# Performance work log

Hardware: AMD Instinct MI355X
Metric: run time of the kernel (lower is better)

The kernel has to match this reference:

```python
import jax, jax.numpy as jnp
import numpy as np

K = 128      # num_topics
T = 256      # num_times
E = 320      # rho_size
H = 10       # num_heads (fixed in source)
HD = E // H  # head dim
TM1 = T - 1
EPS = 1e-5   # nn.LayerNorm default eps


def setup_inputs() -> dict:
    key = jax.random.key(0)
    ks = jax.random.split(key, 6)
    s = 0.02
    return {
        "mu_0_alpha": jax.random.normal(ks[0], (1, K, E), jnp.float32),
        "qkv_w": jax.random.normal(ks[1], (3 * E, E), jnp.float32) * s,
        "qkv_b": jnp.zeros((3 * E,), jnp.float32),
        "in_proj_w": jax.random.normal(ks[2], (3 * E, E), jnp.float32) * s,
        "in_proj_b": jnp.zeros((3 * E,), jnp.float32),
        "out_w": jax.random.normal(ks[3], (E, E), jnp.float32) * s,
        "out_b": jnp.zeros((E,), jnp.float32),
        "ln_g": jnp.ones((E,), jnp.float32),
        "ln_b": jnp.zeros((E,), jnp.float32),
    }


def _layer_norm(x, g, b):
    m = jnp.mean(x, axis=-1, keepdims=True)
    v = jnp.mean((x - m) ** 2, axis=-1, keepdims=True)
    return (x - m) * jax.lax.rsqrt(v + EPS) * g + b


def reference(mu_0_alpha, qkv_w, qkv_b, in_proj_w, in_proj_b, out_w, out_b, ln_g, ln_b):
    # nn.MultiheadAttention in-projection split (q/k/v same embed_dim)
    Wq, Wk, Wv = jnp.split(in_proj_w, 3, axis=0)   # each (E, E)
    bq, bk, bv = jnp.split(in_proj_b, 3, axis=0)
    scale = 1.0 / np.sqrt(HD)

    alpha0 = _layer_norm(mu_0_alpha[0], ln_g, ln_b)  # (K, E)
    kc0 = jnp.zeros((TM1 * K, E), jnp.float32)       # persistent projected-K cache
    vc0 = jnp.zeros((TM1 * K, E), jnp.float32)
    pos = jnp.arange(TM1 * K)

    def step(carry, idx):
        alpha, kc, vc = carry
        # per-step qkv_proj (the module's own Linear, before MHA's in-proj)
        qkv = alpha @ qkv_w.T + qkv_b                 # (K, 3E)
        q, k, v = jnp.split(qkv, 3, axis=-1)
        # MHA in-projections; store projected K/V in the cache (equivalent to
        # projecting the concatenated cache each step, since proj is per-row)
        q2 = (q @ Wq.T + bq) * scale                  # (K, E)
        k2 = k @ Wk.T + bk
        v2 = v @ Wv.T + bv
        kc = jax.lax.dynamic_update_slice(kc, k2, (idx * K, 0))
        vc = jax.lax.dynamic_update_slice(vc, v2, (idx * K, 0))
        qh = q2.reshape(K, H, HD).transpose(1, 0, 2)          # (H, K, HD)
        kh = kc.reshape(TM1 * K, H, HD).transpose(1, 0, 2)    # (H, S, HD)
        vh = vc.reshape(TM1 * K, H, HD).transpose(1, 0, 2)
        scores = jnp.einsum('hqd,hkd->hqk', qh, kh)           # (H, K, S)
        valid = pos < (idx + 1) * K                            # growing-KV mask
        scores = jnp.where(valid[None, None, :], scores, -1e30)
        w = jax.nn.softmax(scores, axis=-1)
        o = jnp.einsum('hqk,hkd->hqd', w, vh)                  # (H, K, HD)
        o = o.transpose(1, 0, 2).reshape(K, E) @ out_w.T + out_b
        new_alpha = _layer_norm(o + alpha, ln_g, ln_b)         # residual + LN
        return (new_alpha, kc, vc), new_alpha

    _, alphas_rest = jax.lax.scan(step, (alpha0, kc0, vc0), jnp.arange(TM1))
    return jnp.concatenate([alpha0[None], alphas_rest], axis=0)  # (T, K, E)
```

## Files before the change

kernel.cpp:

```cpp
#include <hip/hip_runtime.h>
#include <hip/hip_bf16.h>
#include <math.h>

typedef __hip_bfloat16 bf16;
using short4v = __attribute__((ext_vector_type(4))) short;
using short8 = __attribute__((ext_vector_type(8))) short;
using f32x4  = __attribute__((ext_vector_type(4))) float;

#define E_ 320
#define K_ 128
#define H_ 10
#define HD_ 32
#define T_ 256
#define TM1_ 255
#define SMAX_ (TM1_*K_)
#define MAXCH_ 25
#define NBLK_ 256
#define QSCALE 0.17677669529663687f
#define EPS_LN 1e-5f

#define LD1(d,p)  asm volatile("global_load_dword %0, %1, off sc0 sc1"   : "=v"(d) : "v"(p))
#define LD2(d,p)  asm volatile("global_load_dwordx2 %0, %1, off sc0 sc1" : "=v"(d) : "v"(p))
#define LD4(d,p)  asm volatile("global_load_dwordx4 %0, %1, off sc0 sc1" : "=v"(d) : "v"(p))
#define WD1(a)            asm volatile("s_waitcnt vmcnt(0)" : "+v"(a) :: "memory")
#define WD2(a,b)          asm volatile("s_waitcnt vmcnt(0)" : "+v"(a),"+v"(b) :: "memory")
#define WD4(a,b,c,d)      asm volatile("s_waitcnt vmcnt(0)" : "+v"(a),"+v"(b),"+v"(c),"+v"(d) :: "memory")
#define WD8(a,b,c,d,e,f,g,h) asm volatile("s_waitcnt vmcnt(0)" : "+v"(a),"+v"(b),"+v"(c),"+v"(d),"+v"(e),"+v"(f),"+v"(g),"+v"(h) :: "memory")

__device__ __forceinline__ void st_sc_f32(float* p, float v){
  asm volatile("global_store_dword %0, %1, off sc0 sc1" :: "v"(p), "v"(v) : "memory");
}
__device__ __forceinline__ void st_sc_f32x4(float* p, f32x4 v){
  asm volatile("global_store_dwordx4 %0, %1, off sc0 sc1" :: "v"(p), "v"(v) : "memory");
}
__device__ __forceinline__ void st_sc_b64(void* p, short4v v){
  asm volatile("global_store_dwordx2 %0, %1, off sc0 sc1" :: "v"(p), "v"(v) : "memory");
}
__device__ __forceinline__ void st_sc_bf16(bf16* p, float v){
  bf16 b = __float2bfloat16(v);
  unsigned u = *(const unsigned short*)&b;
  asm volatile("global_store_short %0, %1, off sc0 sc1" :: "v"(p), "v"(u) : "memory");
}

__device__ __forceinline__ float ldin(const void* p, size_t i, int isbf){
  if (isbf) return __bfloat162float(((const bf16*)p)[i]);
  return ((const float*)p)[i];
}
__device__ __forceinline__ void stout(void* p, size_t i, float v, int isbf){
  if (isbf) ((bf16*)p)[i] = __float2bfloat16(v);
  else      ((float*)p)[i] = v;
}

__device__ __forceinline__ void reduce2_320(float& a, float& b, float* sc){
  #pragma unroll
  for (int off = 32; off > 0; off >>= 1){
    a += __shfl_down(a, off, 64);
    b += __shfl_down(b, off, 64);
  }
  int w = threadIdx.x >> 6, lane = threadIdx.x & 63;
  __syncthreads();
  if (lane == 0){ sc[w] = a; sc[8+w] = b; }
  __syncthreads();
  a = sc[0]+sc[1]+sc[2]+sc[3]+sc[4];
  b = sc[8]+sc[9]+sc[10]+sc[11]+sc[12];
}

__global__ void detect_kernel(const void* __restrict__ mu0, int* __restrict__ flag,
                              unsigned* bar_cnt, unsigned* bar_gen){
  int lane = threadIdx.x;
  const unsigned short* u = (const unsigned short*)mu0;
  int cnt = 0;
  #pragma unroll
  for (int rep = 0; rep < 2; ++rep){
    unsigned short w = u[(size_t)(lane + rep*64) * 2];
    float v = __uint_as_float(((unsigned int)w) << 16);
    float a = fabsf(v);
    if (a >= 1e-4f && a <= 64.f) cnt++;
  }
  #pragma unroll
  for (int off = 32; off > 0; off >>= 1) cnt += __shfl_down(cnt, off, 64);
  if (lane == 0){
    *flag = (cnt >= 64) ? 1 : 0;
    *bar_cnt = 0u;
    *bar_gen = 0u;
  }
}

__global__ __launch_bounds__(256) void setup_wc(const void* __restrict__ inw,
                                                const void* __restrict__ qkvw,
                                                bf16* __restrict__ WcB,
                                                const int* __restrict__ flagp){
  const int isbf = *flagp;
  int sec = blockIdx.z;
  int i = blockIdx.y*16 + threadIdx.y;
  int o = blockIdx.x*16 + threadIdx.x;
  __shared__ float As[16][17];
  __shared__ float Bs[16][17];
  float acc = 0.f;
  for (int mt = 0; mt < E_; mt += 16){
    As[threadIdx.y][threadIdx.x] = ldin(inw, ((size_t)(sec*E_ + blockIdx.x*16 + threadIdx.x))*E_ + mt + threadIdx.y, isbf);
    Bs[threadIdx.y][threadIdx.x] = ldin(qkvw, ((size_t)(sec*E_ + mt + threadIdx.x))*E_ + blockIdx.y*16 + threadIdx.y, isbf);
    __syncthreads();
    #pragma unroll
    for (int mm = 0; mm < 16; ++mm) acc += Bs[threadIdx.y][mm] * As[mm][threadIdx.x];
    __syncthreads();
  }
  if (sec == 0) acc *= QSCALE;
  WcB[((size_t)(sec*E_ + o))*E_ + i] = __float2bfloat16(acc);
}

__global__ __launch_bounds__(256) void setup_misc(const void* __restrict__ inw,
                                                  const void* __restrict__ inb,
                                                  const void* __restrict__ qkvb,
                                                  const void* __restrict__ outw,
                                                  const void* __restrict__ outb,
                                                  const void* __restrict__ lng,
                                                  const void* __restrict__ lnb,
                                                  float* __restrict__ bc,
                                                  bf16* __restrict__ owB,
                                                  float* __restrict__ vec,
                                                  const int* __restrict__ flagp){
  const int isbf = *flagp;
  int id = blockIdx.x*256 + threadIdx.x;
  if (id < 960){
    int sec = id / E_, o = id % E_;
    float acc = 0.f;
    for (int m = 0; m < E_; ++m)
      acc += ldin(inw, ((size_t)(sec*E_+o))*E_ + m, isbf) * ldin(qkvb, sec*E_ + m, isbf);
    acc += ldin(inb, id, isbf);
    if (sec == 0) acc *= QSCALE;
    bc[id] = acc;
  }
  int j = id - 1024;
  if (j >= 0 && j < E_*E_){
    owB[j] = __float2bfloat16(ldin(outw, j, isbf));
  }
  int v = id - (1024 + E_*E_);
  if (v >= 0 && v < 960){
    if (v < 320)       vec[v] = ldin(outb, v, isbf);
    else if (v < 640)  vec[v] = ldin(lng, v - 320, isbf);
    else               vec[v] = ldin(lnb, v - 640, isbf);
  }
}

__global__ __launch_bounds__(320) void ln0_kernel(const void* __restrict__ mu0,
                                                  const float* __restrict__ vec,
                                                  float* __restrict__ alpha,
                                                  void* __restrict__ out,
                                                  const int* __restrict__ flagp){
  const int isbf = *flagp;
  int r = blockIdx.x, c = threadIdx.x;
  __shared__ float sc[16];
  float x = ldin(mu0, (size_t)r*E_ + c, isbf);
  float s = x, s2 = x*x;
  reduce2_320(s, s2, sc);
  float mean = s * (1.f/E_);
  float var  = s2 * (1.f/E_) - mean*mean;
  float y = (x - mean) * rsqrtf(var + EPS_LN) * vec[320 + c] + vec[640 + c];
  alpha[(size_t)r*E_ + c] = y;
  stout(out, (size_t)r*E_ + c, y, isbf);
}

__device__ __forceinline__ void grid_barrier(unsigned* cnt, unsigned* gen){
  __syncthreads();
  if (threadIdx.x == 0){
    unsigned g = __hip_atomic_load(gen, __ATOMIC_RELAXED, __HIP_MEMORY_SCOPE_AGENT);
    unsigned a = __hip_atomic_fetch_add(cnt, 1u, __ATOMIC_RELAXED, __HIP_MEMORY_SCOPE_AGENT);
    if (a == NBLK_ - 1u){
      __hip_atomic_store(cnt, 0u, __ATOMIC_RELAXED, __HIP_MEMORY_SCOPE_AGENT);
      asm volatile("s_waitcnt vmcnt(0)" ::: "memory");
      __hip_atomic_store(gen, g + 1u, __ATOMIC_RELAXED, __HIP_MEMORY_SCOPE_AGENT);
    } else {
      while (__hip_atomic_load(gen, __ATOMIC_RELAXED, __HIP_MEMORY_SCOPE_AGENT) == g)
        __builtin_amdgcn_s_sleep(8);
    }
  }
  __syncthreads();
}

#define SM_A2   10496
#define SM_C    20992
#define SM_MLL  41984
#define SM_SIZE 42624

__device__ __forceinline__ void cp_phase(int cg, int rg, int t, int nch,
                                         int do_combine, int do_project,
                                         const float* part, const bf16* owB, const bf16* WcB,
                                         const float* bc, const float* vec,
                                         const float* ain, float* aout, void* out, int isbf,
                                         bf16* q2b, bf16* kcb, bf16* vtb, char* smem){
  int tid = threadIdx.x;
  int w = tid >> 6, lane = tid & 63, cn = lane & 15, quad = lane >> 4;
  int r0 = rg*16;
  bf16 (*af)[328]   = (bf16(*)[328])(smem);
  bf16 (*a2)[328]   = (bf16(*)[328])(smem + SM_A2);
  float (*xbuf)[328]= (float(*)[328])(smem + SM_C);
  float (*mlw)[10][26] = (float(*)[10][26])(smem + SM_C);
  float (*mlL)[10]  = (float(*)[10])(smem + SM_MLL);

  if (do_combine){
    if (tid < 160){
      int r = tid / 10, h = tid - 10*(tid/10);
      const float* pb = part + (((size_t)h*MAXCH_)*K_ + r0 + r)*36 + 32;
      float m0=-INFINITY,m1=-INFINITY,m2=-INFINITY,m3=-INFINITY;
      int ci = 0;
      for (; ci + 4 <= nch; ci += 4){
        float t0,t1,t2,t3;
        LD1(t0, pb + (ci+0)*4608); LD1(t1, pb + (ci+1)*4608);
        LD1(t2, pb + (ci+2)*4608); LD1(t3, pb + (ci+3)*4608);
        WD4(t0,t1,t2,t3);
        m0=fmaxf(m0,t0); m1=fmaxf(m1,t1); m2=fmaxf(m2,t2); m3=fmaxf(m3,t3);
      }
      for (; ci < nch; ++ci){ float t0; LD1(t0, pb + ci*4608); WD1(t0); m0=fmaxf(m0,t0); }
      float mst = fmaxf(fmaxf(m0,m1), fmaxf(m2,m3));
      float L0=0.f, L1=0.f, L2=0.f, L3=0.f;
      ci = 0;
      for (; ci + 4 <= nch; ci += 4){
        float2 v0,v1,v2,v3;
        LD2(v0, pb + (ci+0)*4608); LD2(v1, pb + (ci+1)*4608);
        LD2(v2, pb + (ci+2)*4608); LD2(v3, pb + (ci+3)*4608);
        WD4(v0,v1,v2,v3);
        float w0=__expf(v0.x-mst), w1=__expf(v1.x-mst), w2=__expf(v2.x-mst), w3=__expf(v3.x-mst);
        mlw[r][h][ci+0]=w0; mlw[r][h][ci+1]=w1; mlw[r][h][ci+2]=w2; mlw[r][h][ci+3]=w3;
        L0 += w0*v0.y; L1 += w1*v1.y; L2 += w2*v2.y; L3 += w3*v3.y;
      }
      for (; ci < nch; ++ci){
        float2 v0; LD2(v0, pb + ci*4608); WD1(v0);
        float wg = __expf(v0.x - mst);
        mlw[r][h][ci] = wg; L0 += wg*v0.y;
      }
      mlL[r][h] = (L0+L1)+(L2+L3);
    }
    __syncthreads();

    #pragma unroll
    for (int k = 0; k < 5; ++k){
      int e1 = tid + (2*k)*512, e2 = tid + (2*k+1)*512;
      int r1 = e1/320, c1 = e1 - 320*r1, h1 = c1 >> 5, d1 = c1 & 31;
      int r2 = e2/320, c2 = e2 - 320*r2, h2 = c2 >> 5, d2 = c2 & 31;
      const float* p1 = part + (((size_t)h1*MAXCH_)*K_ + r0 + r1)*36 + d1;
      const float* p2 = part + (((size_t)h2*MAXCH_)*K_ + r0 + r2)*36 + d2;
      float a0=0.f,a1=0.f,a2_=0.f,a3=0.f,b0=0.f,b1=0.f,b2=0.f,b3=0.f;
      int ci = 0;
      for (; ci + 4 <= nch; ci += 4){
        float x0,x1,x2,x3,y0,y1,y2,y3;
        LD1(x0, p1+(ci+0)*4608); LD1(x1, p1+(ci+1)*4608);
        LD1(x2, p1+(ci+2)*4608); LD1(x3, p1+(ci+3)*4608);
        LD1(y0, p2+(ci+0)*4608); LD1(y1, p2+(ci+1)*4608);
        LD1(y2, p2+(ci+2)*4608); LD1(y3, p2+(ci+3)*4608);
        WD8(x0,x1,x2,x3,y0,y1,y2,y3);
        a0 += mlw[r1][h1][ci+0]*x0; a1 += mlw[r1][h1][ci+1]*x1;
        a2_+= mlw[r1][h1][ci+2]*x2; a3 += mlw[r1][h1][ci+3]*x3;
        b0 += mlw[r2][h2][ci+0]*y0; b1 += mlw[r2][h2][ci+1]*y1;
        b2 += mlw[r2][h2][ci+2]*y2; b3 += mlw[r2][h2][ci+3]*y3;
      }
      for (; ci < nch; ++ci){
        float x0,y0;
        LD1(x0, p1+ci*4608); LD1(y0, p2+ci*4608);
        WD2(x0,y0);
        a0 += mlw[r1][h1][ci]*x0;
        b0 += mlw[r2][h2][ci]*y0;
      }
      af[r1][c1] = __float2bfloat16(((a0+a1)+(a2_+a3)) / mlL[r1][h1]);
      af[r2][c2] = __float2bfloat16(((b0+b1)+(b2+b3)) / mlL[r2][h2]);
    }
    __syncthreads();

    {
      f32x4 acc[3]; int ntv[3]; int ntc = 0;
      for (int nt = w; nt < 20; nt += 8){ ntv[ntc] = nt; acc[ntc] = (f32x4){0.f,0.f,0.f,0.f}; ntc++; }
      for (int kk = 0; kk < 10; ++kk){
        short8 afr = *(const short8*)(const void*)(&af[cn][kk*32 + quad*8]);
        for (int i = 0; i < ntc; ++i){
          short8 bfr = *(const short8*)(const void*)(owB + ((size_t)(ntv[i]*16 + cn))*E_ + kk*32 + quad*8);
          acc[i] = __builtin_amdgcn_mfma_f32_16x16x32_bf16(afr, bfr, acc[i], 0, 0, 0);
        }
      }
      __syncthreads();
      for (int i = 0; i < ntc; ++i){
        int col = ntv[i]*16 + cn;
        float rv0,rv1,rv2,rv3;
        LD1(rv0, ain + (size_t)(r0+quad*4+0)*E_ + col);
        LD1(rv1, ain + (size_t)(r0+quad*4+1)*E_ + col);
        LD1(rv2, ain + (size_t)(r0+quad*4+2)*E_ + col);
        LD1(rv3, ain + (size_t)(r0+quad*4+3)*E_ + col);
        WD4(rv0,rv1,rv2,rv3);
        float vb = vec[col];
        xbuf[quad*4+0][col] = acc[i][0] + vb + rv0;
        xbuf[quad*4+1][col] = acc[i][1] + vb + rv1;
        xbuf[quad*4+2][col] = acc[i][2] + vb + rv2;
        xbuf[quad*4+3][col] = acc[i][3] + vb + rv3;
      }
    }
    __syncthreads();

    {
      int lr = tid >> 5;
      int j32 = tid & 31;
      float s = 0.f, s2 = 0.f;
      for (int c = j32; c < E_; c += 32){ float x = xbuf[lr][c]; s += x; s2 += x*x; }
      #pragma unroll
      for (int off = 1; off < 32; off <<= 1){
        s  += __shfl_xor(s, off, 32);
        s2 += __shfl_xor(s2, off, 32);
      }
      float mean = s * (1.f/E_);
      float var  = s2 * (1.f/E_) - mean*mean;
      float rs = rsqrtf(var + EPS_LN);
      for (int c = j32; c < E_; c += 32){
        float y = (xbuf[lr][c] - mean) * rs * vec[320 + c] + vec[640 + c];
        a2[lr][c] = __float2bfloat16(y);
        if (cg == 0){
          st_sc_f32(aout + (size_t)(r0+lr)*E_ + c, y);
          stout(out, ((size_t)t*K_ + r0 + lr)*E_ + c, y, isbf);
        }
      }
    }
    __syncthreads();
  } else {
    for (int v = tid; v < 16*E_; v += 512){
      int r = v / E_, e = v - E_*(v/E_);
      float x; LD1(x, ain + (size_t)(r0+r)*E_ + e); WD1(x);
      a2[r][e] = __float2bfloat16(x);
    }
    __syncthreads();
  }

  if (!do_project) return;

  {
    f32x4 acc[3]; int ntv[3]; int ntc = 0;
    for (int nt = w; nt < 20; nt += 8){ ntv[ntc] = nt; acc[ntc] = (f32x4){0.f,0.f,0.f,0.f}; ntc++; }
    for (int kk = 0; kk < 10; ++kk){
      short8 afr = *(const short8*)(const void*)(&a2[cn][kk*32 + quad*8]);
      for (int i = 0; i < ntc; ++i){
        short8 bfr = *(const short8*)(const void*)(WcB + ((size_t)(cg*E_ + ntv[i]*16 + cn))*E_ + kk*32 + quad*8);
        acc[i] = __builtin_amdgcn_mfma_f32_16x16x32_bf16(afr, bfr, acc[i], 0, 0, 0);
      }
    }
    for (int i = 0; i < ntc; ++i){
      int coll = ntv[i]*16 + cn;
      float bias = bc[cg*E_ + coll];
      if (cg == 0){
        #pragma unroll
        for (int rr = 0; rr < 4; ++rr)
          st_sc_bf16(q2b + (size_t)(r0 + quad*4 + rr)*E_ + coll, acc[i][rr] + bias);
      } else if (cg == 1){
        #pragma unroll
        for (int rr = 0; rr < 4; ++rr)
          st_sc_bf16(kcb + ((size_t)(t*K_ + r0 + quad*4 + rr))*E_ + coll, acc[i][rr] + bias);
      } else {
        union { short4v v; bf16 e[4]; } u;
        #pragma unroll
        for (int rr = 0; rr < 4; ++rr) u.e[rr] = __float2bfloat16(acc[i][rr] + bias);
        st_sc_b64(vtb + (size_t)coll*SMAX_ + t*K_ + r0 + quad*4, u.v);
      }
    }
  }
}

__device__ __forceinline__ void attn_cell(int ci, int h, const bf16* q2b, const bf16* kcb,
                                          const bf16* vtb, float* part, int S, int chunkS,
                                          char* smem){
  int w    = threadIdx.x >> 6;
  int lane = threadIdx.x & 63;
  int cn   = lane & 15;
  int quad = lane >> 4;
  bf16 (*pbuf)[40] = (bf16(*)[40])(smem + w*16*40*2);

  int s0 = ci*chunkS, s1 = min(s0 + chunkS, S);

  short8 qf;
  LD4(qf, q2b + (size_t)(w*16 + cn)*E_ + h*HD_ + quad*8);
  WD1(qf);

  f32x4 accT[2];
  accT[0] = (f32x4){0.f,0.f,0.f,0.f};
  accT[1] = (f32x4){0.f,0.f,0.f,0.f};
  float mcol = -INFINITY, lcol = 0.f;

  for (int sb = s0; sb < s1; sb += 32){
    short8 kf0 = *(const short8*)(const void*)(kcb + (size_t)(sb +      cn)*E_ + h*HD_ + quad*8);
    short8 kf1 = *(const short8*)(const void*)(kcb + (size_t)(sb + 16 + cn)*E_ + h*HD_ + quad*8);
    short8 vf0 = *(const short8*)(const void*)(vtb + (size_t)(h*HD_ +      cn)*SMAX_ + sb + quad*8);
    short8 vf1 = *(const short8*)(const void*)(vtb + (size_t)(h*HD_ + 16 + cn)*SMAX_ + sb + quad*8);
    f32x4 z = (f32x4){0.f,0.f,0.f,0.f};
    f32x4 sT0 = __builtin_amdgcn_mfma_f32_16x16x32_bf16(kf0, qf, z, 0, 0, 0);
    f32x4 sT1 = __builtin_amdgcn_mfma_f32_16x16x32_bf16(kf1, qf, z, 0, 0, 0);

    float mx = fmaxf(fmaxf(fmaxf(sT0[0], sT0[1]), fmaxf(sT0[2], sT0[3])),
                     fmaxf(fmaxf(sT1[0], sT1[1]), fmaxf(sT1[2], sT1[3])));
    mx = fmaxf(mx, __shfl_xor(mx, 16, 64));
    mx = fmaxf(mx, __shfl_xor(mx, 32, 64));
    float mn = fmaxf(mcol, mx);
    float corr = __expf(mcol - mn);
    mcol = mn;

    float p0[4], p1[4];
    #pragma unroll
    for (int r = 0; r < 4; ++r){ p0[r] = __expf(sT0[r] - mn); p1[r] = __expf(sT1[r] - mn); }
    float ps = (p0[0]+p0[1]) + (p0[2]+p0[3]) + (p1[0]+p1[1]) + (p1[2]+p1[3]);
    ps += __shfl_xor(ps, 16, 64);
    ps += __shfl_xor(ps, 32, 64);
    lcol = lcol*corr + ps;
    accT[0] *= corr;
    accT[1] *= corr;

    union { short4v v; bf16 e[4]; } u0, u1;
    #pragma unroll
    for (int r = 0; r < 4; ++r){ u0.e[r] = __float2bfloat16(p0[r]); u1.e[r] = __float2bfloat16(p1[r]); }
    *(short4v*)(void*)(&pbuf[cn][quad*4])      = u0.v;
    *(short4v*)(void*)(&pbuf[cn][16 + quad*4]) = u1.v;
    asm volatile("s_waitcnt lgkmcnt(0)" ::: "memory");
    short8 pf = *(const short8*)(const void*)(&pbuf[cn][quad*8]);
    accT[0] = __builtin_amdgcn_mfma_f32_16x16x32_bf16(vf0, pf, accT[0], 0, 0, 0);
    accT[1] = __builtin_amdgcn_mfma_f32_16x16x32_bf16(vf1, pf, accT[1], 0, 0, 0);
  }

  size_t base = (((size_t)h*MAXCH_ + ci)*K_ + 16*w + cn)*36;
  st_sc_f32x4(part + base + quad*4,      accT[0]);
  st_sc_f32x4(part + base + 16 + quad*4, accT[1]);
  if (quad == 0){
    st_sc_f32(part + base + 32, mcol);
    st_sc_f32(part + base + 33, lcol);
  }
}

__global__ __launch_bounds__(512) void mega_kernel(const bf16* WcB, const bf16* owB,
                                                   const float* bc, const float* vec,
                                                   float* abuf0, float* abuf1,
                                                   float* part, const int* flagp,
                                                   bf16* q2b, bf16* kcb, bf16* vtb,
                                                   void* out,
                                                   unsigned* bar_cnt, unsigned* bar_gen){
  __shared__ __align__(16) char smem[SM_SIZE];
  const int isbf = *flagp;
  int b = blockIdx.x;
  int cg = b / 8, rg = b - 8*(b/8);

  int nch_prev = 0;
  for (int t = 0; t < TM1_; ++t){
    const float* ain = (t == 0) ? abuf0 : ((t & 1) ? abuf0 : abuf1);
    float* aout = (t & 1) ? abuf1 : abuf0;
    if (b < 24)
      cp_phase(cg, rg, t, nch_prev, (t > 0) ? 1 : 0, 1,
               part, owB, WcB, bc, vec, ain, aout, out, isbf, q2b, kcb, vtb, smem);
    grid_barrier(bar_cnt, bar_gen);

    int S = (t+1)*K_;
    int nch = (S + 127) / 128; if (nch > MAXCH_) nch = MAXCH_;
    int chunkS = (((S + nch - 1)/nch) + 31) / 32 * 32;
    int nchU = (S + chunkS - 1) / chunkS;
    if (b < nchU*10)
      attn_cell(b/10, b - 10*(b/10), q2b, kcb, vtb, part, S, chunkS, smem);
    grid_barrier(bar_cnt, bar_gen);
    nch_prev = nchU;
  }
  if (b < 8){
    const float* ain = abuf0;
    float* aout = abuf1;
    cp_phase(0, b, TM1_, nch_prev, 1, 0,
             part, owB, WcB, bc, vec, ain, aout, out, isbf, q2b, kcb, vtb, smem);
  }
}

extern "C" void kernel_launch(void* const* d_in, const int* in_sizes, int n_in,
                              void* d_out, int out_size, void* d_ws, size_t ws_size,
                              hipStream_t stream){
  const void* mu0  = d_in[0];
  const void* qkvw = d_in[1];
  const void* qkvb = d_in[2];
  const void* inw  = d_in[3];
  const void* inb  = d_in[4];
  const void* outw = d_in[5];
  const void* outb = d_in[6];
  const void* lng  = d_in[7];
  const void* lnb  = d_in[8];
  float* ws = (float*)d_ws;

  const size_t O_WCB    = 0;
  const size_t O_OWB    = 153600;
  const size_t O_BC     = 204800;
  const size_t O_VEC    = 205824;
  const size_t O_A0     = 206848;
  const size_t O_A1     = 247808;
  const size_t O_PART   = 288768;
  const size_t O_FLAG   = 1440768;
  const size_t O_Q2     = 1440864;
  const size_t O_KC     = 1461344;
  const size_t O_VT     = 6683744;

  bf16*  WcB   = (bf16*)(ws + O_WCB);
  bf16*  owB   = (bf16*)(ws + O_OWB);
  float* bc    = ws + O_BC;
  float* vec   = ws + O_VEC;
  float* abuf0 = ws + O_A0;
  float* abuf1 = ws + O_A1;
  float* part  = ws + O_PART;
  int*   flag  = (int*)(ws + O_FLAG);
  unsigned* bar_cnt = (unsigned*)(ws + O_FLAG + 32);
  unsigned* bar_gen = (unsigned*)(ws + O_FLAG + 64);
  bf16*  q2b   = (bf16*)(ws + O_Q2);
  bf16*  kcb   = (bf16*)(ws + O_KC);
  bf16*  vtb   = (bf16*)(ws + O_VT);

  detect_kernel<<<dim3(1), dim3(64), 0, stream>>>(mu0, flag, bar_cnt, bar_gen);
  setup_wc<<<dim3(20,20,3), dim3(16,16), 0, stream>>>(inw, qkvw, WcB, flag);
  setup_misc<<<dim3(408), dim3(256), 0, stream>>>(inw, inb, qkvb, outw, outb, lng, lnb, bc, owB, vec, flag);
  ln0_kernel<<<dim3(128), dim3(320), 0, stream>>>(mu0, vec, abuf0, d_out, flag);
  mega_kernel<<<dim3(NBLK_), dim3(512), 0, stream>>>(WcB, owB, bc, vec, abuf0, abuf1,
                                                     part, flag, q2b, kcb, vtb, d_out,
                                                     bar_cnt, bar_gen);
}
```

Measured before the change: 17.52 ms.

## Double block size to 1024 threads, split attention chunks across two wave groups

The persistent mega kernel now launches 1024 threads per block. Each attention cell splits its KV tiles between two groups of 8 waves and merges their partial softmax states in shared memory. The KV loop gains register double-buffering of the K/V fragments, the combine, projection and LayerNorm loops are re-indexed for 16 waves, and the barrier spin sleep is shortened. The aim is more memory parallelism per block on the serial per-step critical path, at the cost of higher register pressure and an extra intra-block sync and merge.

```diff
diff --git a/kernel.cpp b/kernel.cpp
--- a/kernel.cpp
+++ b/kernel.cpp
@@ -172,16 +172,17 @@
       __hip_atomic_store(gen, g + 1u, __ATOMIC_RELAXED, __HIP_MEMORY_SCOPE_AGENT);
     } else {
       while (__hip_atomic_load(gen, __ATOMIC_RELAXED, __HIP_MEMORY_SCOPE_AGENT) == g)
-        __builtin_amdgcn_s_sleep(8);
+        __builtin_amdgcn_s_sleep(2);
     }
   }
   __syncthreads();
 }
 
-#define SM_A2   10496
-#define SM_C    20992
-#define SM_MLL  41984
-#define SM_SIZE 42624
+#define SM_A2    10496
+#define SM_C     20992
+#define SM_MLL   41984
+#define SM_MERGE 20480
+#define SM_SIZE  42624
 
 __device__ __forceinline__ void cp_phase(int cg, int rg, int t, int nch,
                                          int do_combine, int do_project,
@@ -190,7 +191,7 @@
                                          const float* ain, float* aout, void* out, int isbf,
                                          bf16* q2b, bf16* kcb, bf16* vtb, char* smem){
   int tid = threadIdx.x;
-  int w = tid >> 6, lane = tid & 63, cn = lane & 15, quad = lane >> 4;
+  int w16 = tid >> 6, lane = tid & 63, cn = lane & 15, quad = lane >> 4;
   int r0 = rg*16;
   bf16 (*af)[328]   = (bf16(*)[328])(smem);
   bf16 (*a2)[328]   = (bf16(*)[328])(smem + SM_A2);
@@ -234,8 +235,8 @@
     __syncthreads();
 
     #pragma unroll
-    for (int k = 0; k < 5; ++k){
-      int e1 = tid + (2*k)*512, e2 = tid + (2*k+1)*512;
+    for (int pp = 0; pp < 2; ++pp){
+      int e1 = tid + (2*pp)*1024, e2 = tid + (2*pp+1)*1024;
       int r1 = e1/320, c1 = e1 - 320*r1, h1 = c1 >> 5, d1 = c1 & 31;
       int r2 = e2/320, c2 = e2 - 320*r2, h2 = c2 >> 5, d2 = c2 & 31;
       const float* p1 = part + (((size_t)h1*MAXCH_)*K_ + r0 + r1)*36 + d1;
@@ -264,11 +265,35 @@
       af[r1][c1] = __float2bfloat16(((a0+a1)+(a2_+a3)) / mlL[r1][h1]);
       af[r2][c2] = __float2bfloat16(((b0+b1)+(b2+b3)) / mlL[r2][h2]);
     }
-    __syncthreads();
-
     {
-      f32x4 acc[3]; int ntv[3]; int ntc = 0;
-      for (int nt = w; nt < 20; nt += 8){ ntv[ntc] = nt; acc[ntc] = (f32x4){0.f,0.f,0.f,0.f}; ntc++; }
+      int e = tid + 4*1024;
+      int r = e/320, c = e - 320*r, h = c >> 5, d = c & 31;
+      const float* p = part + (((size_t)h*MAXCH_)*K_ + r0 + r)*36 + d;
+      float a0=0.f,a1=0.f,a2_=0.f,a3=0.f;
+      int ci = 0;
+      for (; ci + 8 <= nch; ci += 8){
+        float x0,x1,x2,x3,x4,x5,x6,x7;
+        LD1(x0, p+(ci+0)*4608); LD1(x1, p+(ci+1)*4608);
+        LD1(x2, p+(ci+2)*4608); LD1(x3, p+(ci+3)*4608);
+        LD1(x4, p+(ci+4)*4608); LD1(x5, p+(ci+5)*4608);
+        LD1(x6, p+(ci+6)*4608); LD1(x7, p+(ci+7)*4608);
+        WD8(x0,x1,x2,x3,x4,x5,x6,x7);
+        a0 += mlw[r][h][ci+0]*x0; a1 += mlw[r][h][ci+1]*x1;
+        a2_+= mlw[r][h][ci+2]*x2; a3 += mlw[r][h][ci+3]*x3;
+        a0 += mlw[r][h][ci+4]*x4; a1 += mlw[r][h][ci+5]*x5;
+        a2_+= mlw[r][h][ci+6]*x6; a3 += mlw[r][h][ci+7]*x7;
+      }
+      for (; ci < nch; ++ci){
+        float x0; LD1(x0, p+ci*4608); WD1(x0);
+        a0 += mlw[r][h][ci]*x0;
+      }
+      af[r][c] = __float2bfloat16(((a0+a1)+(a2_+a3)) / mlL[r][h]);
+    }
+    __syncthreads();
+
+    {
+      f32x4 acc[2]; int ntv[2]; int ntc = 0;
+      for (int nt = w16; nt < 20; nt += 16){ ntv[ntc] = nt; acc[ntc] = (f32x4){0.f,0.f,0.f,0.f}; ntc++; }
       for (int kk = 0; kk < 10; ++kk){
         short8 afr = *(const short8*)(const void*)(&af[cn][kk*32 + quad*8]);
         for (int i = 0; i < ntc; ++i){
@@ -295,20 +320,27 @@
     __syncthreads();
 
     {
-      int lr = tid >> 5;
-      int j32 = tid & 31;
+      int lr = w16;
+      int j = lane;
+      float xv[5];
       float s = 0.f, s2 = 0.f;
-      for (int c = j32; c < E_; c += 32){ float x = xbuf[lr][c]; s += x; s2 += x*x; }
       #pragma unroll
-      for (int off = 1; off < 32; off <<= 1){
-        s  += __shfl_xor(s, off, 32);
-        s2 += __shfl_xor(s2, off, 32);
+      for (int k = 0; k < 5; ++k){
+        xv[k] = xbuf[lr][j + k*64];
+        s += xv[k]; s2 += xv[k]*xv[k];
+      }
+      #pragma unroll
+      for (int off = 1; off < 64; off <<= 1){
+        s  += __shfl_xor(s, off, 64);
+        s2 += __shfl_xor(s2, off, 64);
       }
       float mean = s * (1.f/E_);
       float var  = s2 * (1.f/E_) - mean*mean;
       float rs = rsqrtf(var + EPS_LN);
-      for (int c = j32; c < E_; c += 32){
-        float y = (xbuf[lr][c] - mean) * rs * vec[320 + c] + vec[640 + c];
+      #pragma unroll
+      for (int k = 0; k < 5; ++k){
+        int c = j + k*64;
+        float y = (xv[k] - mean) * rs * vec[320 + c] + vec[640 + c];
         a2[lr][c] = __float2bfloat16(y);
         if (cg == 0){
           st_sc_f32(aout + (size_t)(r0+lr)*E_ + c, y);
@@ -318,7 +350,7 @@
     }
     __syncthreads();
   } else {
-    for (int v = tid; v < 16*E_; v += 512){
+    for (int v = tid; v < 16*E_; v += 1024){
       int r = v / E_, e = v - E_*(v/E_);
       float x; LD1(x, ain + (size_t)(r0+r)*E_ + e); WD1(x);
       a2[r][e] = __float2bfloat16(x);
@@ -329,8 +361,8 @@
   if (!do_project) return;
 
   {
-    f32x4 acc[3]; int ntv[3]; int ntc = 0;
-    for (int nt = w; nt < 20; nt += 8){ ntv[ntc] = nt; acc[ntc] = (f32x4){0.f,0.f,0.f,0.f}; ntc++; }
+    f32x4 acc[2]; int ntv[2]; int ntc = 0;
+    for (int nt = w16; nt < 20; nt += 16){ ntv[ntc] = nt; acc[ntc] = (f32x4){0.f,0.f,0.f,0.f}; ntc++; }
     for (int kk = 0; kk < 10; ++kk){
       short8 afr = *(const short8*)(const void*)(&a2[cn][kk*32 + quad*8]);
       for (int i = 0; i < ntc; ++i){
@@ -362,16 +394,26 @@
 __device__ __forceinline__ void attn_cell(int ci, int h, const bf16* q2b, const bf16* kcb,
                                           const bf16* vtb, float* part, int S, int chunkS,
                                           char* smem){
-  int w    = threadIdx.x >> 6;
-  int lane = threadIdx.x & 63;
+  int tid  = threadIdx.x;
+  int w16  = tid >> 6;
+  int qt   = w16 & 7;
+  int grp  = w16 >> 3;
+  int lane = tid & 63;
   int cn   = lane & 15;
   int quad = lane >> 4;
-  bf16 (*pbuf)[40] = (bf16(*)[40])(smem + w*16*40*2);
+  bf16 (*pbuf)[40] = (bf16(*)[40])(smem + w16*1280);
+  float* mm = (float*)(smem + SM_MERGE + qt*2176);
+  float* ll = mm + 16;
+  float (*ac)[8] = (float(*)[8])(mm + 32);
 
   int s0 = ci*chunkS, s1 = min(s0 + chunkS, S);
+  int nt = (s1 - s0) >> 5;
+  int nt0 = (nt + 1) >> 1;
+  int tb = grp ? nt0 : 0;
+  int te = grp ? nt : nt0;
 
   short8 qf;
-  LD4(qf, q2b + (size_t)(w*16 + cn)*E_ + h*HD_ + quad*8);
+  LD4(qf, q2b + (size_t)(qt*16 + cn)*E_ + h*HD_ + quad*8);
   WD1(qf);
 
   f32x4 accT[2];
@@ -379,14 +421,30 @@
   accT[1] = (f32x4){0.f,0.f,0.f,0.f};
   float mcol = -INFINITY, lcol = 0.f;
 
-  for (int sb = s0; sb < s1; sb += 32){
-    short8 kf0 = *(const short8*)(const void*)(kcb + (size_t)(sb +      cn)*E_ + h*HD_ + quad*8);
-    short8 kf1 = *(const short8*)(const void*)(kcb + (size_t)(sb + 16 + cn)*E_ + h*HD_ + quad*8);
-    short8 vf0 = *(const short8*)(const void*)(vtb + (size_t)(h*HD_ +      cn)*SMAX_ + sb + quad*8);
-    short8 vf1 = *(const short8*)(const void*)(vtb + (size_t)(h*HD_ + 16 + cn)*SMAX_ + sb + quad*8);
+  const size_t koff = (size_t)h*HD_ + quad*8;
+  const size_t voff = ((size_t)h*HD_ + cn)*SMAX_ + quad*8;
+  const size_t voff2 = ((size_t)h*HD_ + 16 + cn)*SMAX_ + quad*8;
+
+  short8 kc0, kc1, vc0, vc1;
+  if (tb < te){
+    int sb = s0 + (tb << 5);
+    kc0 = *(const short8*)(const void*)(kcb + (size_t)(sb +      cn)*E_ + koff);
+    kc1 = *(const short8*)(const void*)(kcb + (size_t)(sb + 16 + cn)*E_ + koff);
+    vc0 = *(const short8*)(const void*)(vtb + voff  + sb);
+    vc1 = *(const short8*)(const void*)(vtb + voff2 + sb);
+  }
+  for (int ti = tb; ti < te; ++ti){
+    short8 kn0, kn1, vn0, vn1;
+    if (ti + 1 < te){
+      int sbn = s0 + ((ti+1) << 5);
+      kn0 = *(const short8*)(const void*)(kcb + (size_t)(sbn +      cn)*E_ + koff);
+      kn1 = *(const short8*)(const void*)(kcb + (size_t)(sbn + 16 + cn)*E_ + koff);
+      vn0 = *(const short8*)(const void*)(vtb + voff  + sbn);
+      vn1 = *(const short8*)(const void*)(vtb + voff2 + sbn);
+    }
     f32x4 z = (f32x4){0.f,0.f,0.f,0.f};
-    f32x4 sT0 = __builtin_amdgcn_mfma_f32_16x16x32_bf16(kf0, qf, z, 0, 0, 0);
-    f32x4 sT1 = __builtin_amdgcn_mfma_f32_16x16x32_bf16(kf1, qf, z, 0, 0, 0);
+    f32x4 sT0 = __builtin_amdgcn_mfma_f32_16x16x32_bf16(kc0, qf, z, 0, 0, 0);
+    f32x4 sT1 = __builtin_amdgcn_mfma_f32_16x16x32_bf16(kc1, qf, z, 0, 0, 0);
 
     float mx = fmaxf(fmaxf(fmaxf(sT0[0], sT0[1]), fmaxf(sT0[2], sT0[3])),
                      fmaxf(fmaxf(sT1[0], sT1[1]), fmaxf(sT1[2], sT1[3])));
@@ -413,26 +471,46 @@
     *(short4v*)(void*)(&pbuf[cn][16 + quad*4]) = u1.v;
     asm volatile("s_waitcnt lgkmcnt(0)" ::: "memory");
     short8 pf = *(const short8*)(const void*)(&pbuf[cn][quad*8]);
-    accT[0] = __builtin_amdgcn_mfma_f32_16x16x32_bf16(vf0, pf, accT[0], 0, 0, 0);
-    accT[1] = __builtin_amdgcn_mfma_f32_16x16x32_bf16(vf1, pf, accT[1], 0, 0, 0);
-  }
-
-  size_t base = (((size_t)h*MAXCH_ + ci)*K_ + 16*w + cn)*36;
-  st_sc_f32x4(part + base + quad*4,      accT[0]);
-  st_sc_f32x4(part + base + 16 + quad*4, accT[1]);
-  if (quad == 0){
-    st_sc_f32(part + base + 32, mcol);
-    st_sc_f32(part + base + 33, lcol);
-  }
-}
-
-__global__ __launch_bounds__(512) void mega_kernel(const bf16* WcB, const bf16* owB,
-                                                   const float* bc, const float* vec,
-                                                   float* abuf0, float* abuf1,
-                                                   float* part, const int* flagp,
-                                                   bf16* q2b, bf16* kcb, bf16* vtb,
-                                                   void* out,
-                                                   unsigned* bar_cnt, unsigned* bar_gen){
+    accT[0] = __builtin_amdgcn_mfma_f32_16x16x32_bf16(vc0, pf, accT[0], 0, 0, 0);
+    accT[1] = __builtin_amdgcn_mfma_f32_16x16x32_bf16(vc1, pf, accT[1], 0, 0, 0);
+
+    kc0 = kn0; kc1 = kn1; vc0 = vn0; vc1 = vn1;
+  }
+
+  if (grp == 1){
+    if (quad == 0){ mm[cn] = mcol; ll[cn] = lcol; }
+    #pragma unroll
+    for (int r = 0; r < 4; ++r){ ac[lane][r] = accT[0][r]; ac[lane][4+r] = accT[1][r]; }
+  }
+  __syncthreads();
+  if (grp == 0){
+    float m1 = mm[cn], l1 = ll[cn];
+    float ms = fmaxf(mcol, m1);
+    float c0 = __expf(mcol - ms), c1 = __expf(m1 - ms);
+    float lv = lcol*c0 + l1*c1;
+    f32x4 o0, o1;
+    #pragma unroll
+    for (int r = 0; r < 4; ++r){
+      o0[r] = accT[0][r]*c0 + ac[lane][r]*c1;
+      o1[r] = accT[1][r]*c0 + ac[lane][4+r]*c1;
+    }
+    size_t base = (((size_t)h*MAXCH_ + ci)*K_ + 16*qt + cn)*36;
+    st_sc_f32x4(part + base + quad*4,      o0);
+    st_sc_f32x4(part + base + 16 + quad*4, o1);
+    if (quad == 0){
+      st_sc_f32(part + base + 32, ms);
+      st_sc_f32(part + base + 33, lv);
+    }
+  }
+}
+
+__global__ __launch_bounds__(1024) void mega_kernel(const bf16* WcB, const bf16* owB,
+                                                    const float* bc, const float* vec,
+                                                    float* abuf0, float* abuf1,
+                                                    float* part, const int* flagp,
+                                                    bf16* q2b, bf16* kcb, bf16* vtb,
+                                                    void* out,
+                                                    unsigned* bar_cnt, unsigned* bar_gen){
   __shared__ __align__(16) char smem[SM_SIZE];
   const int isbf = *flagp;
   int b = blockIdx.x;
@@ -508,7 +586,7 @@
   setup_wc<<<dim3(20,20,3), dim3(16,16), 0, stream>>>(inw, qkvw, WcB, flag);
   setup_misc<<<dim3(408), dim3(256), 0, stream>>>(inw, inb, qkvb, outw, outb, lng, lnb, bc, owB, vec, flag);
   ln0_kernel<<<dim3(128), dim3(320), 0, stream>>>(mu0, vec, abuf0, d_out, flag);
-  mega_kernel<<<dim3(NBLK_), dim3(512), 0, stream>>>(WcB, owB, bc, vec, abuf0, abuf1,
-                                                     part, flag, q2b, kcb, vtb, d_out,
-                                                     bar_cnt, bar_gen);
-}
+  mega_kernel<<<dim3(NBLK_), dim3(1024), 0, stream>>>(WcB, owB, bc, vec, abuf0, abuf1,
+                                                      part, flag, q2b, kcb, vtb, d_out,
+                                                      bar_cnt, bar_gen);
+}
```

New measurement: 17.84 ms. Within noise of the previous version (+1.8%).
